# Kernel optimization log

Measured on AMD Instinct MI355X. Metric: run time of the kernel, lower is better.

## Reference

```python
import jax, jax.numpy as jnp
import numpy as np

D_MODEL = 1024
NUM_HEADS = 16
D_K = D_MODEL // NUM_HEADS


def setup_inputs() -> dict:
    key = jax.random.key(0)
    ks = jax.random.split(key, 9)
    B, S = 2, 2048
    scale = 1.0 / np.sqrt(D_MODEL)
    x = jax.random.normal(ks[0], (B, S, D_MODEL), dtype=jnp.float32)
    Wq = jax.random.normal(ks[1], (D_MODEL, D_MODEL), dtype=jnp.float32) * scale
    Wk = jax.random.normal(ks[2], (D_MODEL, D_MODEL), dtype=jnp.float32) * scale
    Wv = jax.random.normal(ks[3], (D_MODEL, D_MODEL), dtype=jnp.float32) * scale
    Wo = jax.random.normal(ks[4], (D_MODEL, D_MODEL), dtype=jnp.float32) * scale
    bq = jax.random.normal(ks[5], (D_MODEL,), dtype=jnp.float32) * 0.01
    bk = jax.random.normal(ks[6], (D_MODEL,), dtype=jnp.float32) * 0.01
    bv = jax.random.normal(ks[7], (D_MODEL,), dtype=jnp.float32) * 0.01
    bo = jax.random.normal(ks[8], (D_MODEL,), dtype=jnp.float32) * 0.01
    return {"x": x, "Wq": Wq, "bq": bq, "Wk": Wk, "bk": bk,
            "Wv": Wv, "bv": bv, "Wo": Wo, "bo": bo}


def reference(x, Wq, bq, Wk, bk, Wv, bv, Wo, bo):
    B, S, _ = x.shape
    H, Dk = NUM_HEADS, D_K
    # projections -> [B, H, S, Dk]
    def split_heads(t):
        return t.reshape(B, S, H, Dk).transpose(0, 2, 1, 3)
    q = split_heads(x @ Wq + bq)
    k = split_heads(x @ Wk + bk)
    v = split_heads(x @ Wv + bv)
    # full score matrix [B, H, S, S] (faithful to the original non-fused impl)
    scores = jnp.einsum('bhqd,bhkd->bhqk', q, k) / jnp.sqrt(jnp.float32(Dk))
    attn = jax.nn.softmax(scores, axis=-1)
    out = jnp.einsum('bhqk,bhkd->bhqd', attn, v)
    out = out.transpose(0, 2, 1, 3).reshape(B, S, H * Dk)
    return out @ Wo + bo
```

## Files before the change

### kernel.cpp

```cpp
#include <hip/hip_runtime.h>
#include <cstdint>

constexpr int S    = 2048;
constexpr int D    = 1024;
constexpr int NH   = 16;
constexpr int DK   = 64;
constexpr int MTOK = 2 * S;

typedef __bf16 bf16x8 __attribute__((ext_vector_type(8)));
typedef __bf16 bf16x4 __attribute__((ext_vector_type(4)));
typedef float  floatx4 __attribute__((ext_vector_type(4)));

__device__ __forceinline__ void async_cp16(const void* g, void* l) {
    __builtin_amdgcn_global_load_lds(
        (const __attribute__((address_space(1))) uint32_t*)g,
        (__attribute__((address_space(3))) uint32_t*)l, 16, 0, 0);
}

__global__ __launch_bounds__(256) void cvt_prep(
    const float* __restrict__ x, __bf16* __restrict__ xb,
    const float* __restrict__ W0, const float* __restrict__ W1,
    const float* __restrict__ W2, const float* __restrict__ W3,
    __bf16* __restrict__ T0, __bf16* __restrict__ T1,
    __bf16* __restrict__ T2, __bf16* __restrict__ T3)
{
    const int t = threadIdx.x;
    if (blockIdx.z == 4) {
        int blk = blockIdx.y * 16 + blockIdx.x;
        const float4* src = (const float4*)x;
        #pragma unroll
        for (int ii = 0; ii < 16; ++ii) {
            int idx = blk * 4096 + ii * 256 + t;
            float4 v = src[idx];
            bf16x4 o;
            o[0] = (__bf16)v.x; o[1] = (__bf16)v.y; o[2] = (__bf16)v.z; o[3] = (__bf16)v.w;
            *(bf16x4*)&xb[(size_t)idx * 4] = o;
        }
        return;
    }
    const float* W = (blockIdx.z == 0) ? W0 : (blockIdx.z == 1) ? W1 : (blockIdx.z == 2) ? W2 : W3;
    __bf16*      T = (blockIdx.z == 0) ? T0 : (blockIdx.z == 1) ? T1 : (blockIdx.z == 2) ? T2 : T3;
    __shared__ __bf16 tile[64][65];
    const int k0 = blockIdx.y * 64, n0 = blockIdx.x * 64;
    #pragma unroll
    for (int i = 0; i < 4; ++i) {
        int k = (t >> 4) + i * 16;
        int n = (t & 15) * 4;
        float4 v = *(const float4*)&W[(size_t)(k0 + k) * D + n0 + n];
        tile[n + 0][k] = (__bf16)v.x;
        tile[n + 1][k] = (__bf16)v.y;
        tile[n + 2][k] = (__bf16)v.z;
        tile[n + 3][k] = (__bf16)v.w;
    }
    __syncthreads();
    #pragma unroll
    for (int i = 0; i < 4; ++i) {
        int n = (t >> 4) + i * 16;
        int k = (t & 15) * 4;
        bf16x4 o;
        o[0] = tile[n][k]; o[1] = tile[n][k + 1]; o[2] = tile[n][k + 2]; o[3] = tile[n][k + 3];
        *(bf16x4*)&T[(size_t)(n0 + n) * D + k0 + k] = o;
    }
}

constexpr int BM = 128, BK = 64;

template<int JT>
__device__ __forceinline__ void gemm_core(
    const __bf16* __restrict__ A, const __bf16* __restrict__ Bt,
    __bf16* Alds, __bf16* Blds, int m0, int n0, floatx4 (&acc)[4][JT])
{
    const int tid = threadIdx.x;
    const int w = tid >> 6, l = tid & 63;
    const int wm = (w >> 1) * 64, wn = (w & 1) * 16 * JT;
    const int lr = l & 15, lg = l >> 4;

    #pragma unroll
    for (int i = 0; i < 4; ++i)
        #pragma unroll
        for (int j = 0; j < JT; ++j)
            acc[i][j] = (floatx4){0.f, 0.f, 0.f, 0.f};

    for (int k0 = 0; k0 < D; k0 += BK) {
        #pragma unroll
        for (int i = 0; i < 4; ++i) {
            int c = i * 256 + tid, row = c >> 3, g = c & 7;
            async_cp16(&A[(size_t)(m0 + row) * D + k0 + g * 8], &Alds[c * 8]);
        }
        #pragma unroll
        for (int i = 0; i < JT; ++i) {
            int c = i * 256 + tid, row = c >> 3, g = c & 7;
            async_cp16(&Bt[(size_t)(n0 + row) * D + k0 + g * 8], &Blds[c * 8]);
        }
        __syncthreads();
        #pragma unroll
        for (int kk = 0; kk < 2; ++kk) {
            bf16x8 af[4], bfr[JT];
            #pragma unroll
            for (int i = 0; i < 4; ++i)
                af[i] = *(const bf16x8*)&Alds[(wm + i * 16 + lr) * BK + kk * 32 + lg * 8];
            #pragma unroll
            for (int j = 0; j < JT; ++j)
                bfr[j] = *(const bf16x8*)&Blds[(wn + j * 16 + lr) * BK + kk * 32 + lg * 8];
            #pragma unroll
            for (int i = 0; i < 4; ++i)
                #pragma unroll
                for (int j = 0; j < JT; ++j)
                    acc[i][j] = __builtin_amdgcn_mfma_f32_16x16x32_bf16(af[i], bfr[j], acc[i][j], 0, 0, 0);
        }
        __syncthreads();
    }
}

__global__ __launch_bounds__(256, 2) void gemm_qkv(
    const __bf16* __restrict__ xb,
    const __bf16* __restrict__ WqT, const __bf16* __restrict__ WkT, const __bf16* __restrict__ WvT,
    const float* __restrict__ bq, const float* __restrict__ bk, const float* __restrict__ bv,
    __bf16* __restrict__ Qb, __bf16* __restrict__ Kb, __bf16* __restrict__ Vt)
{
    __shared__ __align__(16) __bf16 Alds[BM * BK];
    __shared__ __align__(16) __bf16 Blds[128 * BK];
    const int z = blockIdx.z;
    const __bf16* Bt   = (z == 0) ? WqT : (z == 1) ? WkT : WvT;
    const float*  bias = (z == 0) ? bq : (z == 1) ? bk : bv;
    const int m0 = blockIdx.y * BM, n0 = blockIdx.x * 128;

    floatx4 acc[4][4];
    gemm_core<4>(xb, Bt, Alds, Blds, m0, n0, acc);

    const int tid = threadIdx.x;
    const int w = tid >> 6, l = tid & 63;
    const int wm = (w >> 1) * 64, wn = (w & 1) * 64;
    const int lr = l & 15, lg = l >> 4;

    if (z == 0) {
        const float scale = 0.18033688f;
        #pragma unroll
        for (int i = 0; i < 4; ++i)
            #pragma unroll
            for (int j = 0; j < 4; ++j) {
                int n = n0 + wn + j * 16 + lr;
                #pragma unroll
                for (int r = 0; r < 4; ++r) {
                    int m = m0 + wm + i * 16 + lg * 4 + r;
                    float v = (acc[i][j][r] + bias[n]) * scale;
                    size_t off = ((size_t)((m >> 11) * NH + (n >> 6)) * S + (m & (S - 1))) * DK + (n & (DK - 1));
                    Qb[off] = (__bf16)v;
                }
            }
    } else if (z == 1) {
        #pragma unroll
        for (int i = 0; i < 4; ++i)
            #pragma unroll
            for (int j = 0; j < 4; ++j) {
                int n = n0 + wn + j * 16 + lr;
                int dk = n & 63;
                float bn = bias[n];
                #pragma unroll
                for (int r = 0; r < 4; ++r) {
                    int m = m0 + wm + i * 16 + lg * 4 + r;
                    int s = m & (S - 1);
                    int bhh = (m >> 11) * NH + (n >> 6);
                    size_t off = (size_t)bhh * S * DK + (size_t)(s >> 6) * 4096
                               + (s & 63) * 64 + (((dk >> 3) ^ (s & 7)) * 8) + (dk & 7);
                    Kb[off] = (__bf16)(acc[i][j][r] + bn);
                }
            }
    } else {
        #pragma unroll
        for (int i = 0; i < 4; ++i)
            #pragma unroll
            for (int j = 0; j < 4; ++j) {
                int n = n0 + wn + j * 16 + lr;
                int dk = n & 63;
                int m = m0 + wm + i * 16 + lg * 4;
                int s = m & (S - 1);
                int bhh = (m >> 11) * NH + (n >> 6);
                float bn = bias[n];
                bf16x4 o;
                #pragma unroll
                for (int r = 0; r < 4; ++r) o[r] = (__bf16)(acc[i][j][r] + bn);
                size_t off = (size_t)bhh * DK * S + (size_t)(s >> 6) * 4096
                           + dk * 64 + ((((s >> 3) & 7) ^ (dk & 7)) * 8) + (s & 7);
                *(bf16x4*)&Vt[off] = o;
            }
    }
}

__global__ __launch_bounds__(256, 2) void gemm_out(
    const __bf16* __restrict__ A, const __bf16* __restrict__ Bt,
    const float* __restrict__ bias, float* __restrict__ Cout)
{
    __shared__ __align__(16) __bf16 Alds[BM * BK];
    __shared__ __align__(16) __bf16 Blds[64 * BK];
    const int m0 = blockIdx.y * BM, n0 = blockIdx.x * 64;

    floatx4 acc[4][2];
    gemm_core<2>(A, Bt, Alds, Blds, m0, n0, acc);

    const int tid = threadIdx.x;
    const int w = tid >> 6, l = tid & 63;
    const int wm = (w >> 1) * 64, wn = (w & 1) * 32;
    const int lr = l & 15, lg = l >> 4;
    #pragma unroll
    for (int i = 0; i < 4; ++i)
        #pragma unroll
        for (int j = 0; j < 2; ++j) {
            int n = n0 + wn + j * 16 + lr;
            #pragma unroll
            for (int r = 0; r < 4; ++r) {
                int m = m0 + wm + i * 16 + lg * 4 + r;
                Cout[(size_t)m * D + n] = acc[i][j][r] + bias[n];
            }
        }
}

constexpr int QT = 128;
constexpr int KT = 64;
constexpr float SOFTMAX_C2 = 14.4269504f;

__global__ __launch_bounds__(256, 2) void attn_mfma(
    const __bf16* __restrict__ Q, const __bf16* __restrict__ Kswz,
    const __bf16* __restrict__ Vswz, __bf16* __restrict__ O)
{
    __shared__ __align__(16) __bf16 Klds[2][KT * DK];
    __shared__ __align__(16) __bf16 Vlds[2][DK * KT];
    __shared__ __align__(16) __bf16 Plds[4][32 * 64];

    const int tid = threadIdx.x;
    const int w = tid >> 6, l = tid & 63;
    const int lr = l & 15, lg = l >> 4;
    const int sw = lr & 7;
    const int bh = blockIdx.y;
    const int q0 = blockIdx.x * QT;
    const __bf16* Kb = Kswz + (size_t)bh * S * DK;
    const __bf16* Vb = Vswz + (size_t)bh * DK * S;

    bf16x8 qf[2][2];
    {
        const __bf16* qp = Q + ((size_t)bh * S + q0 + w * 32) * DK;
        #pragma unroll
        for (int i = 0; i < 2; ++i)
            #pragma unroll
            for (int kk = 0; kk < 2; ++kk)
                qf[i][kk] = *(const bf16x8*)&qp[(i * 16 + lr) * DK + kk * 32 + lg * 8];
    }
    bf16x8 vones;
    #pragma unroll
    for (int j = 0; j < 8; ++j) vones[j] = (__bf16)1.0f;

    floatx4 acc[4][2];
    #pragma unroll
    for (int jd = 0; jd < 4; ++jd)
        #pragma unroll
        for (int i = 0; i < 2; ++i)
            acc[jd][i] = (floatx4){0.f, 0.f, 0.f, 0.f};
    floatx4 psacc[2];
    psacc[0] = (floatx4){0.f, 0.f, 0.f, 0.f};
    psacc[1] = (floatx4){0.f, 0.f, 0.f, 0.f};

    auto issue = [&](int tile, int buf) {
        const __bf16* ks = Kb + (size_t)tile * 4096;
        const __bf16* vs = Vb + (size_t)tile * 4096;
        #pragma unroll
        for (int ii = 0; ii < 2; ++ii) {
            int c = ii * 256 + tid;
            async_cp16(&ks[c * 8], &Klds[buf][c * 8]);
            async_cp16(&vs[c * 8], &Vlds[buf][c * 8]);
        }
    };

    issue(0, 0);
    asm volatile("s_waitcnt vmcnt(0)" ::: "memory");

    for (int t0 = 0; t0 < S; t0 += KT) {
        const int tt = t0 >> 6;
        const int cur = tt & 1;
        __syncthreads();
        if (t0 + KT < S) issue(tt + 1, cur ^ 1);

        floatx4 sa[4][2];
        #pragma unroll
        for (int j = 0; j < 4; ++j)
            #pragma unroll
            for (int i = 0; i < 2; ++i)
                sa[j][i] = (floatx4){-SOFTMAX_C2, -SOFTMAX_C2, -SOFTMAX_C2, -SOFTMAX_C2};
        __builtin_amdgcn_s_setprio(1);
        #pragma unroll
        for (int kk = 0; kk < 2; ++kk) {
            bf16x8 kf[4];
            #pragma unroll
            for (int j = 0; j < 4; ++j)
                kf[j] = *(const bf16x8*)&Klds[cur][(j * 16 + lr) * DK + (((kk * 4 + lg) ^ sw) * 8)];
            #pragma unroll
            for (int j = 0; j < 4; ++j)
                #pragma unroll
                for (int i = 0; i < 2; ++i)
                    sa[j][i] = __builtin_amdgcn_mfma_f32_16x16x32_bf16(kf[j], qf[i][kk], sa[j][i], 0, 0, 0);
        }
        __builtin_amdgcn_s_setprio(0);

        #pragma unroll
        for (int j = 0; j < 4; ++j)
            #pragma unroll
            for (int i = 0; i < 2; ++i) {
                bf16x4 pb;
                #pragma unroll
                for (int r = 0; r < 4; ++r)
                    pb[r] = (__bf16)__builtin_amdgcn_exp2f(sa[j][i][r]);
                int gsw = (j * 2 + (lg >> 1)) ^ sw;
                *(bf16x4*)&Plds[w][(i * 16 + lr) * 64 + gsw * 8 + (lg & 1) * 4] = pb;
            }

        __builtin_amdgcn_s_setprio(1);
        #pragma unroll
        for (int kk = 0; kk < 2; ++kk) {
            bf16x8 vf[4], pf[2];
            #pragma unroll
            for (int i = 0; i < 2; ++i) {
                int gsw = (kk * 4 + lg) ^ sw;
                pf[i] = *(const bf16x8*)&Plds[w][(i * 16 + lr) * 64 + gsw * 8];
            }
            #pragma unroll
            for (int jd = 0; jd < 4; ++jd)
                vf[jd] = *(const bf16x8*)&Vlds[cur][(jd * 16 + lr) * KT + (((kk * 4 + lg) ^ sw) * 8)];
            #pragma unroll
            for (int jd = 0; jd < 4; ++jd)
                #pragma unroll
                for (int i = 0; i < 2; ++i)
                    acc[jd][i] = __builtin_amdgcn_mfma_f32_16x16x32_bf16(vf[jd], pf[i], acc[jd][i], 0, 0, 0);
            #pragma unroll
            for (int i = 0; i < 2; ++i)
                psacc[i] = __builtin_amdgcn_mfma_f32_16x16x32_bf16(vones, pf[i], psacc[i], 0, 0, 0);
        }
        __builtin_amdgcn_s_setprio(0);

        asm volatile("s_waitcnt vmcnt(0)" ::: "memory");
    }

    const int b = bh >> 4, h = bh & 15;
    #pragma unroll
    for (int i = 0; i < 2; ++i) {
        float inv = 1.f / psacc[i][0];
        int q = q0 + w * 32 + i * 16 + lr;
        __bf16* op = O + (size_t)(b * S + q) * D + h * DK;
        #pragma unroll
        for (int jd = 0; jd < 4; ++jd) {
            bf16x4 ov;
            #pragma unroll
            for (int r = 0; r < 4; ++r) ov[r] = (__bf16)(acc[jd][i][r] * inv);
            *(bf16x4*)&op[jd * 16 + lg * 4] = ov;
        }
    }
}

extern "C" void kernel_launch(void* const* d_in, const int* in_sizes, int n_in,
                              void* d_out, int out_size, void* d_ws, size_t ws_size,
                              hipStream_t stream) {
    const float* x  = (const float*)d_in[0];
    const float* Wq = (const float*)d_in[1];
    const float* bq = (const float*)d_in[2];
    const float* Wk = (const float*)d_in[3];
    const float* bk = (const float*)d_in[4];
    const float* Wv = (const float*)d_in[5];
    const float* bv = (const float*)d_in[6];
    const float* Wo = (const float*)d_in[7];
    const float* bo = (const float*)d_in[8];

    char* ws = (char*)d_ws;
    __bf16* xb  = (__bf16*)(ws);
    __bf16* WqT = (__bf16*)(ws + (8ull  << 20));
    __bf16* WkT = (__bf16*)(ws + (10ull << 20));
    __bf16* WvT = (__bf16*)(ws + (12ull << 20));
    __bf16* WoT = (__bf16*)(ws + (14ull << 20));
    __bf16* Qb  = (__bf16*)(ws + (16ull << 20));
    __bf16* Kb  = (__bf16*)(ws + (24ull << 20));
    __bf16* Vt  = (__bf16*)(ws + (32ull << 20));
    __bf16* Ob  = (__bf16*)(ws + (40ull << 20));

    cvt_prep<<<dim3(16, 16, 5), 256, 0, stream>>>(
        x, xb, Wq, Wk, Wv, Wo, WqT, WkT, WvT, WoT);

    gemm_qkv<<<dim3(D / 128, MTOK / BM, 3), 256, 0, stream>>>(
        xb, WqT, WkT, WvT, bq, bk, bv, Qb, Kb, Vt);

    attn_mfma<<<dim3(S / QT, 2 * NH), 256, 0, stream>>>(Qb, Kb, Vt, Ob);

    gemm_out<<<dim3(D / 64, MTOK / BM), 256, 0, stream>>>(Ob, WoT, bo, (float*)d_out);
}
```

Measured before the change: 191.2 us.

## Split attention warps across query and key halves with end-of-loop LDS reduction

```diff
diff --git a/kernel.cpp b/kernel.cpp
--- a/kernel.cpp
+++ b/kernel.cpp
@@ -223,24 +223,26 @@
     const __bf16* __restrict__ Q, const __bf16* __restrict__ Kswz,
     const __bf16* __restrict__ Vswz, __bf16* __restrict__ O)
 {
-    __shared__ __align__(16) __bf16 Klds[2][KT * DK];
-    __shared__ __align__(16) __bf16 Vlds[2][DK * KT];
-    __shared__ __align__(16) __bf16 Plds[4][32 * 64];
+    __shared__ __align__(16) char smem[49664];
+    __bf16 (*Klds)[KT * DK] = (__bf16 (*)[KT * DK])smem;
+    __bf16 (*Vlds)[DK * KT] = (__bf16 (*)[DK * KT])(smem + 16384);
 
     const int tid = threadIdx.x;
     const int w = tid >> 6, l = tid & 63;
+    const int wq = w >> 1, wk = w & 1;
     const int lr = l & 15, lg = l >> 4;
     const int sw = lr & 7;
     const int bh = blockIdx.y;
     const int q0 = blockIdx.x * QT;
     const __bf16* Kb = Kswz + (size_t)bh * S * DK;
     const __bf16* Vb = Vswz + (size_t)bh * DK * S;
-
-    bf16x8 qf[2][2];
+    __bf16* Pw = (__bf16*)(smem + 32768) + w * 2048;
+
+    bf16x8 qf[4][2];
     {
-        const __bf16* qp = Q + ((size_t)bh * S + q0 + w * 32) * DK;
-        #pragma unroll
-        for (int i = 0; i < 2; ++i)
+        const __bf16* qp = Q + ((size_t)bh * S + q0 + wq * 64) * DK;
+        #pragma unroll
+        for (int i = 0; i < 4; ++i)
             #pragma unroll
             for (int kk = 0; kk < 2; ++kk)
                 qf[i][kk] = *(const bf16x8*)&qp[(i * 16 + lr) * DK + kk * 32 + lg * 8];
@@ -249,15 +251,15 @@
     #pragma unroll
     for (int j = 0; j < 8; ++j) vones[j] = (__bf16)1.0f;
 
-    floatx4 acc[4][2];
+    floatx4 acc[4][4];
     #pragma unroll
     for (int jd = 0; jd < 4; ++jd)
         #pragma unroll
-        for (int i = 0; i < 2; ++i)
+        for (int i = 0; i < 4; ++i)
             acc[jd][i] = (floatx4){0.f, 0.f, 0.f, 0.f};
-    floatx4 psacc[2];
-    psacc[0] = (floatx4){0.f, 0.f, 0.f, 0.f};
-    psacc[1] = (floatx4){0.f, 0.f, 0.f, 0.f};
+    floatx4 psacc[4];
+    #pragma unroll
+    for (int i = 0; i < 4; ++i) psacc[i] = (floatx4){0.f, 0.f, 0.f, 0.f};
 
     auto issue = [&](int tile, int buf) {
         const __bf16* ks = Kb + (size_t)tile * 4096;
@@ -279,58 +281,55 @@
         __syncthreads();
         if (t0 + KT < S) issue(tt + 1, cur ^ 1);
 
-        floatx4 sa[4][2];
-        #pragma unroll
-        for (int j = 0; j < 4; ++j)
-            #pragma unroll
-            for (int i = 0; i < 2; ++i)
+        floatx4 sa[2][4];
+        #pragma unroll
+        for (int j = 0; j < 2; ++j)
+            #pragma unroll
+            for (int i = 0; i < 4; ++i)
                 sa[j][i] = (floatx4){-SOFTMAX_C2, -SOFTMAX_C2, -SOFTMAX_C2, -SOFTMAX_C2};
         __builtin_amdgcn_s_setprio(1);
         #pragma unroll
         for (int kk = 0; kk < 2; ++kk) {
-            bf16x8 kf[4];
-            #pragma unroll
-            for (int j = 0; j < 4; ++j)
-                kf[j] = *(const bf16x8*)&Klds[cur][(j * 16 + lr) * DK + (((kk * 4 + lg) ^ sw) * 8)];
-            #pragma unroll
-            for (int j = 0; j < 4; ++j)
-                #pragma unroll
-                for (int i = 0; i < 2; ++i)
+            bf16x8 kf[2];
+            #pragma unroll
+            for (int j = 0; j < 2; ++j)
+                kf[j] = *(const bf16x8*)&Klds[cur][(wk * 32 + j * 16 + lr) * DK + (((kk * 4 + lg) ^ sw) * 8)];
+            #pragma unroll
+            for (int j = 0; j < 2; ++j)
+                #pragma unroll
+                for (int i = 0; i < 4; ++i)
                     sa[j][i] = __builtin_amdgcn_mfma_f32_16x16x32_bf16(kf[j], qf[i][kk], sa[j][i], 0, 0, 0);
         }
         __builtin_amdgcn_s_setprio(0);
 
         #pragma unroll
-        for (int j = 0; j < 4; ++j)
-            #pragma unroll
-            for (int i = 0; i < 2; ++i) {
+        for (int j = 0; j < 2; ++j)
+            #pragma unroll
+            for (int i = 0; i < 4; ++i) {
                 bf16x4 pb;
                 #pragma unroll
                 for (int r = 0; r < 4; ++r)
                     pb[r] = (__bf16)__builtin_amdgcn_exp2f(sa[j][i][r]);
-                int gsw = (j * 2 + (lg >> 1)) ^ sw;
-                *(bf16x4*)&Plds[w][(i * 16 + lr) * 64 + gsw * 8 + (lg & 1) * 4] = pb;
+                int g = (j * 2 + (lg >> 1)) ^ (lr & 3);
+                *(bf16x4*)&Pw[(i * 16 + lr) * 32 + g * 8 + (lg & 1) * 4] = pb;
             }
 
         __builtin_amdgcn_s_setprio(1);
-        #pragma unroll
-        for (int kk = 0; kk < 2; ++kk) {
-            bf16x8 vf[4], pf[2];
-            #pragma unroll
-            for (int i = 0; i < 2; ++i) {
-                int gsw = (kk * 4 + lg) ^ sw;
-                pf[i] = *(const bf16x8*)&Plds[w][(i * 16 + lr) * 64 + gsw * 8];
-            }
+        {
+            bf16x8 vf[4], pf[4];
+            #pragma unroll
+            for (int i = 0; i < 4; ++i)
+                pf[i] = *(const bf16x8*)&Pw[(i * 16 + lr) * 32 + ((lg ^ (lr & 3)) * 8)];
             #pragma unroll
             for (int jd = 0; jd < 4; ++jd)
-                vf[jd] = *(const bf16x8*)&Vlds[cur][(jd * 16 + lr) * KT + (((kk * 4 + lg) ^ sw) * 8)];
+                vf[jd] = *(const bf16x8*)&Vlds[cur][(jd * 16 + lr) * KT + (((wk * 4 + lg) ^ sw) * 8)];
             #pragma unroll
             for (int jd = 0; jd < 4; ++jd)
                 #pragma unroll
-                for (int i = 0; i < 2; ++i)
+                for (int i = 0; i < 4; ++i)
                     acc[jd][i] = __builtin_amdgcn_mfma_f32_16x16x32_bf16(vf[jd], pf[i], acc[jd][i], 0, 0, 0);
             #pragma unroll
-            for (int i = 0; i < 2; ++i)
+            for (int i = 0; i < 4; ++i)
                 psacc[i] = __builtin_amdgcn_mfma_f32_16x16x32_bf16(vones, pf[i], psacc[i], 0, 0, 0);
         }
         __builtin_amdgcn_s_setprio(0);
@@ -338,18 +337,37 @@
         asm volatile("s_waitcnt vmcnt(0)" ::: "memory");
     }
 
-    const int b = bh >> 4, h = bh & 15;
-    #pragma unroll
-    for (int i = 0; i < 2; ++i) {
-        float inv = 1.f / psacc[i][0];
-        int q = q0 + w * 32 + i * 16 + lr;
-        __bf16* op = O + (size_t)(b * S + q) * D + h * DK;
-        #pragma unroll
-        for (int jd = 0; jd < 4; ++jd) {
-            bf16x4 ov;
-            #pragma unroll
-            for (int r = 0; r < 4; ++r) ov[r] = (__bf16)(acc[jd][i][r] * inv);
-            *(bf16x4*)&op[jd * 16 + lg * 4] = ov;
+    __syncthreads();
+    float* red   = (float*)smem;
+    float* psred = (float*)(smem + 36864);
+    if (wk == 1) {
+        #pragma unroll
+        for (int jd = 0; jd < 4; ++jd)
+            #pragma unroll
+            for (int i = 0; i < 4; ++i)
+                *(floatx4*)&red[(wq * 64 + i * 16 + lr) * 72 + jd * 16 + lg * 4] = acc[jd][i];
+        if (lg == 0) {
+            #pragma unroll
+            for (int i = 0; i < 4; ++i)
+                psred[wq * 64 + i * 16 + lr] = psacc[i][0];
+        }
+    }
+    __syncthreads();
+    if (wk == 0) {
+        const int b = bh >> 4, h = bh & 15;
+        #pragma unroll
+        for (int i = 0; i < 4; ++i) {
+            float inv = 1.f / (psacc[i][0] + psred[wq * 64 + i * 16 + lr]);
+            int q = q0 + wq * 64 + i * 16 + lr;
+            __bf16* op = O + (size_t)(b * S + q) * D + h * DK;
+            #pragma unroll
+            for (int jd = 0; jd < 4; ++jd) {
+                floatx4 part = *(const floatx4*)&red[(wq * 64 + i * 16 + lr) * 72 + jd * 16 + lg * 4];
+                bf16x4 ov;
+                #pragma unroll
+                for (int r = 0; r < 4; ++r) ov[r] = (__bf16)((acc[jd][i][r] + part[r]) * inv);
+                *(bf16x4*)&op[jd * 16 + lg * 4] = ov;
+            }
         }
     }
 }
```

Result: no change. 194.1 us (+1.5%).

## Split attention KV range across two blocks and keep P in registers

Applied to the files above, without the earlier changes.

```diff
diff --git a/kernel.cpp b/kernel.cpp
--- a/kernel.cpp
+++ b/kernel.cpp
@@ -10,11 +10,32 @@
 typedef __bf16 bf16x8 __attribute__((ext_vector_type(8)));
 typedef __bf16 bf16x4 __attribute__((ext_vector_type(4)));
 typedef float  floatx4 __attribute__((ext_vector_type(4)));
+typedef unsigned uintx4 __attribute__((ext_vector_type(4)));
+typedef _Float16 halfx4 __attribute__((ext_vector_type(4)));
 
 __device__ __forceinline__ void async_cp16(const void* g, void* l) {
     __builtin_amdgcn_global_load_lds(
         (const __attribute__((address_space(1))) uint32_t*)g,
         (__attribute__((address_space(3))) uint32_t*)l, 16, 0, 0);
+}
+
+__device__ __forceinline__ void swap_rows32(unsigned &a, unsigned &b) {
+#if __has_builtin(__builtin_amdgcn_permlane32_swap)
+    typedef unsigned u32x2 __attribute__((ext_vector_type(2)));
+    u32x2 r = __builtin_amdgcn_permlane32_swap(a, b, false, false);
+    a = r[0]; b = r[1];
+#else
+    asm volatile("v_permlane32_swap_b32 %0, %1" : "+v"(a), "+v"(b));
+#endif
+}
+__device__ __forceinline__ void swap_rows16(unsigned &a, unsigned &b) {
+#if __has_builtin(__builtin_amdgcn_permlane16_swap)
+    typedef unsigned u32x2 __attribute__((ext_vector_type(2)));
+    u32x2 r = __builtin_amdgcn_permlane16_swap(a, b, false, false);
+    a = r[0]; b = r[1];
+#else
+    asm volatile("v_permlane16_swap_b32 %0, %1" : "+v"(a), "+v"(b));
+#endif
 }
 
 __global__ __launch_bounds__(256) void cvt_prep(
@@ -219,19 +240,29 @@
 constexpr int KT = 64;
 constexpr float SOFTMAX_C2 = 14.4269504f;
 
-__global__ __launch_bounds__(256, 2) void attn_mfma(
+__device__ __forceinline__ unsigned pkexp2(float a, float b) {
+    float lo = __builtin_amdgcn_exp2f(a);
+    float hi = __builtin_amdgcn_exp2f(b);
+    unsigned r;
+    asm("v_cvt_pk_bf16_f32 %0, %1, %2" : "=v"(r) : "v"(lo), "v"(hi));
+    return r;
+}
+
+__global__ __launch_bounds__(256, 4) void attn_mfma(
     const __bf16* __restrict__ Q, const __bf16* __restrict__ Kswz,
-    const __bf16* __restrict__ Vswz, __bf16* __restrict__ O)
+    const __bf16* __restrict__ Vswz, _Float16* __restrict__ P0,
+    _Float16* __restrict__ P1, __bf16* __restrict__ Ofin,
+    float* __restrict__ Sp, int* __restrict__ flags)
 {
     __shared__ __align__(16) __bf16 Klds[2][KT * DK];
     __shared__ __align__(16) __bf16 Vlds[2][DK * KT];
-    __shared__ __align__(16) __bf16 Plds[4][32 * 64];
 
     const int tid = threadIdx.x;
     const int w = tid >> 6, l = tid & 63;
     const int lr = l & 15, lg = l >> 4;
     const int sw = lr & 7;
     const int bh = blockIdx.y;
+    const int kz = blockIdx.z;
     const int q0 = blockIdx.x * QT;
     const __bf16* Kb = Kswz + (size_t)bh * S * DK;
     const __bf16* Vb = Vswz + (size_t)bh * DK * S;
@@ -270,14 +301,15 @@
         }
     };
 
-    issue(0, 0);
+    const int tbeg = kz * (S / (2 * KT));
+    const int tend = tbeg + (S / (2 * KT));
+    issue(tbeg, 0);
     asm volatile("s_waitcnt vmcnt(0)" ::: "memory");
 
-    for (int t0 = 0; t0 < S; t0 += KT) {
-        const int tt = t0 >> 6;
-        const int cur = tt & 1;
+    for (int tt = tbeg; tt < tend; ++tt) {
+        const int cur = (tt - tbeg) & 1;
         __syncthreads();
-        if (t0 + KT < S) issue(tt + 1, cur ^ 1);
+        if (tt + 1 < tend) issue(tt + 1, cur ^ 1);
 
         floatx4 sa[4][2];
         #pragma unroll
@@ -300,27 +332,26 @@
         }
         __builtin_amdgcn_s_setprio(0);
 
-        #pragma unroll
-        for (int j = 0; j < 4; ++j)
-            #pragma unroll
-            for (int i = 0; i < 2; ++i) {
-                bf16x4 pb;
-                #pragma unroll
-                for (int r = 0; r < 4; ++r)
-                    pb[r] = (__bf16)__builtin_amdgcn_exp2f(sa[j][i][r]);
-                int gsw = (j * 2 + (lg >> 1)) ^ sw;
-                *(bf16x4*)&Plds[w][(i * 16 + lr) * 64 + gsw * 8 + (lg & 1) * 4] = pb;
+        bf16x8 pfr[2][2];
+        #pragma unroll
+        for (int i = 0; i < 2; ++i)
+            #pragma unroll
+            for (int kk = 0; kk < 2; ++kk) {
+                const int j0 = kk * 2, j1 = j0 + 1;
+                unsigned pa = pkexp2(sa[j0][i][0], sa[j0][i][1]);
+                unsigned pc = pkexp2(sa[j0][i][2], sa[j0][i][3]);
+                unsigned pb = pkexp2(sa[j1][i][0], sa[j1][i][1]);
+                unsigned pd = pkexp2(sa[j1][i][2], sa[j1][i][3]);
+                swap_rows32(pa, pb); swap_rows16(pa, pb);
+                swap_rows32(pc, pd); swap_rows16(pc, pd);
+                uintx4 pw = {pa, pc, pb, pd};
+                pfr[kk][i] = __builtin_bit_cast(bf16x8, pw);
             }
 
         __builtin_amdgcn_s_setprio(1);
         #pragma unroll
         for (int kk = 0; kk < 2; ++kk) {
-            bf16x8 vf[4], pf[2];
-            #pragma unroll
-            for (int i = 0; i < 2; ++i) {
-                int gsw = (kk * 4 + lg) ^ sw;
-                pf[i] = *(const bf16x8*)&Plds[w][(i * 16 + lr) * 64 + gsw * 8];
-            }
+            bf16x8 vf[4];
             #pragma unroll
             for (int jd = 0; jd < 4; ++jd)
                 vf[jd] = *(const bf16x8*)&Vlds[cur][(jd * 16 + lr) * KT + (((kk * 4 + lg) ^ sw) * 8)];
@@ -328,10 +359,10 @@
             for (int jd = 0; jd < 4; ++jd)
                 #pragma unroll
                 for (int i = 0; i < 2; ++i)
-                    acc[jd][i] = __builtin_amdgcn_mfma_f32_16x16x32_bf16(vf[jd], pf[i], acc[jd][i], 0, 0, 0);
+                    acc[jd][i] = __builtin_amdgcn_mfma_f32_16x16x32_bf16(vf[jd], pfr[kk][i], acc[jd][i], 0, 0, 0);
             #pragma unroll
             for (int i = 0; i < 2; ++i)
-                psacc[i] = __builtin_amdgcn_mfma_f32_16x16x32_bf16(vones, pf[i], psacc[i], 0, 0, 0);
+                psacc[i] = __builtin_amdgcn_mfma_f32_16x16x32_bf16(vones, pfr[kk][i], psacc[i], 0, 0, 0);
         }
         __builtin_amdgcn_s_setprio(0);
 
@@ -339,17 +370,47 @@
     }
 
     const int b = bh >> 4, h = bh & 15;
+    _Float16* Omine = kz ? P1 : P0;
     #pragma unroll
     for (int i = 0; i < 2; ++i) {
-        float inv = 1.f / psacc[i][0];
         int q = q0 + w * 32 + i * 16 + lr;
-        __bf16* op = O + (size_t)(b * S + q) * D + h * DK;
+        _Float16* op = Omine + (size_t)(b * S + q) * D + h * DK;
         #pragma unroll
         for (int jd = 0; jd < 4; ++jd) {
-            bf16x4 ov;
-            #pragma unroll
-            for (int r = 0; r < 4; ++r) ov[r] = (__bf16)(acc[jd][i][r] * inv);
-            *(bf16x4*)&op[jd * 16 + lg * 4] = ov;
+            halfx4 ov;
+            #pragma unroll
+            for (int r = 0; r < 4; ++r) ov[r] = (_Float16)acc[jd][i][r];
+            *(halfx4*)&op[jd * 16 + lg * 4] = ov;
+        }
+        if (lg == 0)
+            Sp[kz * 32 * S + bh * S + q] = psacc[i][0];
+    }
+    __threadfence();
+    __shared__ int role;
+    __syncthreads();
+    if (tid == 0)
+        role = __hip_atomic_fetch_add(&flags[bh * 16 + blockIdx.x], 1,
+                                      __ATOMIC_ACQ_REL, __HIP_MEMORY_SCOPE_AGENT);
+    __syncthreads();
+    if (role == 1) {
+        __threadfence();
+        const _Float16* Oo = kz ? P0 : P1;
+        const float* SpO = Sp + (kz ^ 1) * 32 * S;
+        #pragma unroll
+        for (int i = 0; i < 2; ++i) {
+            int q = q0 + w * 32 + i * 16 + lr;
+            float inv = 1.f / (psacc[i][0] + SpO[bh * S + q]);
+            const _Float16* opo = Oo + (size_t)(b * S + q) * D + h * DK;
+            __bf16* of = Ofin + (size_t)(b * S + q) * D + h * DK;
+            #pragma unroll
+            for (int jd = 0; jd < 4; ++jd) {
+                halfx4 pv = *(const halfx4*)&opo[jd * 16 + lg * 4];
+                bf16x4 ov;
+                #pragma unroll
+                for (int r = 0; r < 4; ++r)
+                    ov[r] = (__bf16)((acc[jd][i][r] + (float)pv[r]) * inv);
+                *(bf16x4*)&of[jd * 16 + lg * 4] = ov;
+            }
         }
     }
 }
@@ -368,15 +429,19 @@
     const float* bo = (const float*)d_in[8];
 
     char* ws = (char*)d_ws;
-    __bf16* xb  = (__bf16*)(ws);
-    __bf16* WqT = (__bf16*)(ws + (8ull  << 20));
-    __bf16* WkT = (__bf16*)(ws + (10ull << 20));
-    __bf16* WvT = (__bf16*)(ws + (12ull << 20));
-    __bf16* WoT = (__bf16*)(ws + (14ull << 20));
-    __bf16* Qb  = (__bf16*)(ws + (16ull << 20));
-    __bf16* Kb  = (__bf16*)(ws + (24ull << 20));
-    __bf16* Vt  = (__bf16*)(ws + (32ull << 20));
-    __bf16* Ob  = (__bf16*)(ws + (40ull << 20));
+    __bf16*   xb  = (__bf16*)(ws);
+    __bf16*   WqT = (__bf16*)(ws + (8ull  << 20));
+    __bf16*   WkT = (__bf16*)(ws + (10ull << 20));
+    __bf16*   WvT = (__bf16*)(ws + (12ull << 20));
+    __bf16*   Qb  = (__bf16*)(ws + (16ull << 20));
+    __bf16*   Kb  = (__bf16*)(ws + (24ull << 20));
+    __bf16*   Vt  = (__bf16*)(ws + (32ull << 20));
+    __bf16*   WoT = (__bf16*)(ws + (40ull << 20));
+    float*    Sp  = (float*)(ws + (42ull << 20));
+    int*      flg = (int*)(ws + (43ull << 20));
+    _Float16* P0  = (_Float16*)(ws);
+    _Float16* P1  = (_Float16*)(ws + (8ull << 20));
+    __bf16*   Ofn = (__bf16*)(ws);
 
     cvt_prep<<<dim3(16, 16, 5), 256, 0, stream>>>(
         x, xb, Wq, Wk, Wv, Wo, WqT, WkT, WvT, WoT);
@@ -384,7 +449,9 @@
     gemm_qkv<<<dim3(D / 128, MTOK / BM, 3), 256, 0, stream>>>(
         xb, WqT, WkT, WvT, bq, bk, bv, Qb, Kb, Vt);
 
-    attn_mfma<<<dim3(S / QT, 2 * NH), 256, 0, stream>>>(Qb, Kb, Vt, Ob);
-
-    gemm_out<<<dim3(D / 64, MTOK / BM), 256, 0, stream>>>(Ob, WoT, bo, (float*)d_out);
-}
+    hipMemsetAsync(flg, 0, 512 * sizeof(int), stream);
+
+    attn_mfma<<<dim3(S / QT, 2 * NH, 2), 256, 0, stream>>>(Qb, Kb, Vt, P0, P1, Ofn, Sp, flg);
+
+    gemm_out<<<dim3(D / 64, MTOK / BM), 256, 0, stream>>>(Ofn, WoT, bo, (float*)d_out);
+}
```

Measured after the change: 403.3 us. 2.11x slower.
